# Optimization experiments

Hardware: AMD Instinct MI355X
Metric: run time of the kernel (lower is better)

## Reference

```python
import jax, jax.numpy as jnp
import numpy as np

B, L, K, S, D, H, C = 32, 256, 50, 16, 128, 4, 128
V, NN, NU, NS = 50000, 100000, 50000, 5000


def mha(q, k, v, in_w, in_b, out_w, out_b, n_heads):
    # PyTorch nn.MultiheadAttention (batch_first, eval mode) semantics.
    d = q.shape[-1]
    hd = d // n_heads
    wq, wk, wv = jnp.split(in_w, 3, axis=0)
    bq, bk, bv = jnp.split(in_b, 3)
    def heads(t):
        return t.reshape(t.shape[:-1] + (n_heads, hd))
    qh = heads(q @ wq.T + bq)
    kh = heads(k @ wk.T + bk)
    vh = heads(v @ wv.T + bv)
    scores = jnp.einsum('...qhd,...khd->...hqk', qh, kh) / jnp.sqrt(jnp.asarray(hd, q.dtype))
    attn = jax.nn.softmax(scores, axis=-1)
    o = jnp.einsum('...hqk,...khd->...qhd', attn, vh)
    o = o.reshape(o.shape[:-2] + (d,))
    return o @ out_w.T + out_b


def conv1d(x, w, b):
    # x: [B, D, L], w: [Cout, D, k]
    y = jax.lax.conv_general_dilated(x, w, (1,), 'VALID', dimension_numbers=('NCH', 'OIH', 'NCH'))
    return y + b[None, :, None]


def meta_path_module(paths, gru_wih, gru_whh, gru_bih, gru_bhh, in_w, in_b, out_w, out_b, ln_g, ln_b):
    # paths: [B, S, T, D] -> [B, D]
    b, s, t, d = paths.shape
    x = paths.reshape(b * s, t, d)
    def step(h, xt):
        gi = xt @ gru_wih.T + gru_bih
        gh = h @ gru_whh.T + gru_bhh
        ir, iz, inn = jnp.split(gi, 3, axis=-1)
        hr, hz, hn = jnp.split(gh, 3, axis=-1)
        r = jax.nn.sigmoid(ir + hr)
        z = jax.nn.sigmoid(iz + hz)
        n = jnp.tanh(inn + r * hn)
        return (1.0 - z) * n + z * h, None
    h0 = jnp.zeros((b * s, d), paths.dtype)
    h, _ = jax.lax.scan(step, h0, jnp.swapaxes(x, 0, 1))
    enc = h.reshape(b, s, d)
    attn = mha(enc, enc, enc, in_w, in_b, out_w, out_b, H)
    y = enc + attn
    mu = jnp.mean(y, -1, keepdims=True)
    var = jnp.var(y, -1, keepdims=True)
    y = (y - mu) / jnp.sqrt(var + 1e-5) * ln_g + ln_b
    return jnp.mean(y, axis=1)


def _forward(word_table, news_table, user_table, source_table,
             wa_in_w, wa_in_b, wa_out_w, wa_out_b,
             conv_w3, conv_b3, conv_w4, conv_b4, conv_w5, conv_b5, fc_w, fc_b,
             nsn_gru_wih, nsn_gru_whh, nsn_gru_bih, nsn_gru_bhh,
             nsn_in_w, nsn_in_b, nsn_out_w, nsn_out_b, nsn_ln_g, nsn_ln_b,
             nun_gru_wih, nun_gru_whh, nun_gru_bih, nun_gru_bhh,
             nun_in_w, nun_in_b, nun_out_w, nun_out_b, nun_ln_g, nun_ln_b,
             mp_w1, mp_b1, mp_w2, mp_b2, cls_w1, cls_b1, cls_w2, cls_b2,
             news_ids, news_word_indices, word_ctx_ids, nsn_src, nsn_end, nun_usr, nun_end):
    # --- fine-grained word embeds: per-token query attending over context news ---
    base = word_table[news_word_indices]              # [B, L, D]
    ctx = news_table[word_ctx_ids]                    # [B, L, K, D] (dominant gather)
    q = base[:, :, None, :]                           # [B, L, 1, D]
    fine = mha(q, ctx, ctx, wa_in_w, wa_in_b, wa_out_w, wa_out_b, H)[:, :, 0, :]
    pad = (news_word_indices == 0)[..., None]
    doc = jnp.where(pad, jnp.zeros((), base.dtype), fine)   # padding_idx=0 -> zeros
    # --- coarse CNN encoder ---
    x = jnp.swapaxes(doc, 1, 2)                       # [B, D, L]
    pooled = [jnp.max(jax.nn.relu(conv1d(x, w, b)), axis=2)
              for w, b in ((conv_w3, conv_b3), (conv_w4, conv_b4), (conv_w5, conv_b5))]
    semantic = jnp.concatenate(pooled, axis=1) @ fc_w.T + fc_b   # [B, D]
    # --- meta-path interaction ---
    start = jnp.broadcast_to(news_table[news_ids][:, None, :], (B, S, D))
    nsn_paths = jnp.stack([start, source_table[nsn_src], news_table[nsn_end]], axis=2)
    nun_paths = jnp.stack([start, user_table[nun_usr], news_table[nun_end]], axis=2)
    nsn_e = meta_path_module(nsn_paths, nsn_gru_wih, nsn_gru_whh, nsn_gru_bih, nsn_gru_bhh,
                             nsn_in_w, nsn_in_b, nsn_out_w, nsn_out_b, nsn_ln_g, nsn_ln_b)
    nun_e = meta_path_module(nun_paths, nun_gru_wih, nun_gru_whh, nun_gru_bih, nun_gru_bhh,
                             nun_in_w, nun_in_b, nun_out_w, nun_out_b, nun_ln_g, nun_ln_b)
    stack = jnp.stack([nsn_e, nun_e], axis=1)         # [B, 2, D]
    sc = jnp.tanh(stack @ mp_w1.T + mp_b1) @ mp_w2.T + mp_b2
    w = jax.nn.softmax(sc, axis=1)
    struct = jnp.sum(stack * w, axis=1)
    comb = jnp.concatenate([semantic, struct], axis=1)
    hcls = jax.nn.relu(comb @ cls_w1.T + cls_b1)
    return hcls @ cls_w2.T + cls_b2                   # [B, 2]


def setup_inputs() -> dict:
    key = jax.random.key(0)
    ks = iter(jax.random.split(key, 80))
    def p(shape):
        return (jax.random.normal(next(ks), shape, jnp.float32) * 0.02)
    inp = {}
    inp['news_ids'] = jax.random.randint(next(ks), (B,), 0, NN)
    inp['news_word_indices'] = jax.random.randint(next(ks), (B, L), 0, V)
    inp['word_ctx_ids'] = jax.random.randint(next(ks), (B, L, K), 0, NN)
    inp['nsn_src'] = jax.random.randint(next(ks), (B, S), 0, NS)
    inp['nsn_end'] = jax.random.randint(next(ks), (B, S), 0, NN)
    inp['nun_usr'] = jax.random.randint(next(ks), (B, S), 0, NU)
    inp['nun_end'] = jax.random.randint(next(ks), (B, S), 0, NN)
    inp['word_table'] = p((V, D)).at[0].set(0.0)
    inp['news_table'] = p((NN, D))
    inp['user_table'] = p((NU, D))
    inp['source_table'] = p((NS, D))
    inp['wa_in_w'] = p((3 * D, D)); inp['wa_in_b'] = p((3 * D,))
    inp['wa_out_w'] = p((D, D)); inp['wa_out_b'] = p((D,))
    for k in (3, 4, 5):
        inp[f'conv_w{k}'] = p((C, D, k)); inp[f'conv_b{k}'] = p((C,))
    inp['fc_w'] = p((D, 3 * C)); inp['fc_b'] = p((D,))
    for pre in ('nsn', 'nun'):
        inp[f'{pre}_gru_wih'] = p((3 * D, D)); inp[f'{pre}_gru_whh'] = p((3 * D, D))
        inp[f'{pre}_gru_bih'] = p((3 * D,)); inp[f'{pre}_gru_bhh'] = p((3 * D,))
        inp[f'{pre}_in_w'] = p((3 * D, D)); inp[f'{pre}_in_b'] = p((3 * D,))
        inp[f'{pre}_out_w'] = p((D, D)); inp[f'{pre}_out_b'] = p((D,))
        inp[f'{pre}_ln_g'] = jnp.ones((D,), jnp.float32); inp[f'{pre}_ln_b'] = jnp.zeros((D,), jnp.float32)
    inp['mp_w1'] = p((D // 2, D)); inp['mp_b1'] = p((D // 2,))
    inp['mp_w2'] = p((1, D // 2)); inp['mp_b2'] = p((1,))
    inp['cls_w1'] = p((D, 2 * D)); inp['cls_b1'] = p((D,))
    inp['cls_w2'] = p((2, D)); inp['cls_b2'] = p((2,))
    return inp


def reference(word_table, news_table, user_table, source_table,
              wa_in_w, wa_in_b, wa_out_w, wa_out_b,
              conv_w3, conv_b3, conv_w4, conv_b4, conv_w5, conv_b5, fc_w, fc_b,
              nsn_gru_wih, nsn_gru_whh, nsn_gru_bih, nsn_gru_bhh,
              nsn_in_w, nsn_in_b, nsn_out_w, nsn_out_b, nsn_ln_g, nsn_ln_b,
              nun_gru_wih, nun_gru_whh, nun_gru_bih, nun_gru_bhh,
              nun_in_w, nun_in_b, nun_out_w, nun_out_b, nun_ln_g, nun_ln_b,
              mp_w1, mp_b1, mp_w2, mp_b2, cls_w1, cls_b1, cls_w2, cls_b2,
              news_ids, news_word_indices, word_ctx_ids, nsn_src, nsn_end, nun_usr, nun_end):
    return _forward(word_table, news_table, user_table, source_table,
                    wa_in_w, wa_in_b, wa_out_w, wa_out_b,
                    conv_w3, conv_b3, conv_w4, conv_b4, conv_w5, conv_b5, fc_w, fc_b,
                    nsn_gru_wih, nsn_gru_whh, nsn_gru_bih, nsn_gru_bhh,
                    nsn_in_w, nsn_in_b, nsn_out_w, nsn_out_b, nsn_ln_g, nsn_ln_b,
                    nun_gru_wih, nun_gru_whh, nun_gru_bih, nun_gru_bhh,
                    nun_in_w, nun_in_b, nun_out_w, nun_out_b, nun_ln_g, nun_ln_b,
                    mp_w1, mp_b1, mp_w2, mp_b2, cls_w1, cls_b1, cls_w2, cls_b2,
                    news_ids, news_word_indices, word_ctx_ids, nsn_src, nsn_end, nun_usr, nun_end)
```

## Files before the change

### kernel.cpp

```cpp
#include <hip/hip_runtime.h>
#include <hip/hip_bf16.h>

#define BB 32
#define LL 256
#define KC 50
#define SS 16
#define DD 128
#define NH 4
#define CC 128
#define VV 50000
#define NNN 100000
#define NUU 50000
#define NSS 5000

typedef __attribute__((ext_vector_type(8))) short bf16x8;
typedef __attribute__((ext_vector_type(8))) unsigned short u16x8;
typedef __attribute__((ext_vector_type(4))) float f32x4;

__device__ __forceinline__ float dot4(float4 a, float4 b){
  return a.x*b.x + a.y*b.y + a.z*b.z + a.w*b.w;
}

__device__ __forceinline__ unsigned short f2bf(float f){
  union { float f; unsigned int u; } v; v.f = f;
  unsigned int r = (v.u + 0x7FFFu + ((v.u >> 16) & 1u)) >> 16;
  return (unsigned short)r;
}
__device__ __forceinline__ float bf2f(unsigned short s){
  union { unsigned int u; float f; } v; v.u = ((unsigned int)s) << 16;
  return v.f;
}

__global__ __launch_bounds__(256) void k_prep(
    const float* __restrict__ w3, const float* __restrict__ w4,
    const float* __restrict__ w5,
    const float* __restrict__ wih0, const float* __restrict__ whh0,
    const float* __restrict__ wih1, const float* __restrict__ whh1,
    const float* __restrict__ in_w, const float* __restrict__ out_w,
    const float* __restrict__ inw0, const float* __restrict__ outw0,
    const float* __restrict__ inw1, const float* __restrict__ outw1,
    unsigned short* __restrict__ wb3, unsigned short* __restrict__ wb4,
    unsigned short* __restrict__ wb5, unsigned short* __restrict__ wgb,
    unsigned short* __restrict__ wab, unsigned short* __restrict__ wmh){
  int e = blockIdx.x*256 + threadIdx.x;
  if (e < CC*DD*3){ int c=e/(DD*3), rm=e%(DD*3), d=rm/3, jj=rm%3;
    wb3[((size_t)jj*CC + c)*DD + d] = f2bf(w3[e]); }
  if (e < CC*DD*4){ int c=e/(DD*4), rm=e%(DD*4), d=rm/4, jj=rm%4;
    wb4[((size_t)jj*CC + c)*DD + d] = f2bf(w4[e]); }
  if (e < CC*DD*5){ int c=e/(DD*5), rm=e%(DD*5), d=rm/5, jj=rm%5;
    wb5[((size_t)jj*CC + c)*DD + d] = f2bf(w5[e]); }
  if (e < 384*DD){
    wgb[e]          = f2bf(wih0[e]);
    wgb[49152 + e]  = f2bf(whh0[e]);
    wgb[98304 + e]  = f2bf(wih1[e]);
    wgb[147456 + e] = f2bf(whh1[e]);
    wab[e]          = f2bf(in_w[e]);
  }
  if (e >= 384*DD && e < 512*DD) wab[e] = f2bf(out_w[e - 384*DD]);
  if (e < 512*DD){
    float s0 = (e < 384*DD) ? inw0[e] : outw0[e - 384*DD];
    float s1 = (e < 384*DD) ? inw1[e] : outw1[e - 384*DD];
    wmh[e]                 = f2bf(s0);
    wmh[(size_t)512*DD + e] = f2bf(s1);
  }
}

#define F1_GRU 128
#define F1_PKV 1250
#define PST 136
#define TST 72
#define CPAD 136
#define GSTR 392
__global__ __launch_bounds__(256) void k_fused1(
    const float* __restrict__ news, const unsigned short* __restrict__ wkvb,
    const float* __restrict__ in_b,
    unsigned short* __restrict__ nK, unsigned short* __restrict__ nV,
    const float* __restrict__ word_table, const int* __restrict__ widx,
    const unsigned short* __restrict__ wqb, float* __restrict__ qh_out,
    const float* __restrict__ user_table, const float* __restrict__ source_table,
    const int* __restrict__ news_ids, const int* __restrict__ nsn_src,
    const int* __restrict__ nsn_end, const int* __restrict__ nun_usr,
    const int* __restrict__ nun_end, const unsigned short* __restrict__ wgb,
    const float* __restrict__ bih0, const float* __restrict__ bhh0,
    const float* __restrict__ bih1, const float* __restrict__ bhh1,
    float* __restrict__ enc){
  __shared__ __align__(16) char smem[38912];
  const int blk = blockIdx.x;
  const int tid = threadIdx.x;
  const int wave = tid >> 6, lane = tid & 63, l15 = lane & 15, quad = lane >> 4;

  if (blk < F1_GRU){
    auto xs = (unsigned short(*)[CPAD])(smem);
    auto hs = (unsigned short(*)[CPAD])(smem + 4352);
    auto hf = (float(*)[128])(smem + 8704);
    auto gi = (float(*)[GSTR])(smem + 12800);
    auto gh = (float(*)[GSTR])(smem + 25344);
    const int m  = blk >> 6;
    const int b  = (blk >> 1) & 31;
    const int s0 = (blk & 1) * 8;
    const unsigned short* Wih = wgb + (size_t)m*2*384*DD;
    const unsigned short* Whh = Wih + 384*DD;
    const float* bih = m ? bih1 : bih0;
    const float* bhh = m ? bhh1 : bhh0;
    for (int i=tid;i<16*CPAD;i+=256){ (&xs[0][0])[i]=0; (&hs[0][0])[i]=0; }
    for (int i=tid;i<8*128;i+=256) (&hf[0][0])[i]=0.f;
    __syncthreads();
    for (int t=0;t<3;t++){
      {
        int s = tid >> 5, j = tid & 31;
        int row; const float* tab;
        if (t==0){ row = news_ids[b]; tab = news; }
        else if (t==1){ row = m ? nun_usr[b*SS+s0+s] : nsn_src[b*SS+s0+s];
                        tab = m ? user_table : source_table; }
        else { row = m ? nun_end[b*SS+s0+s] : nsn_end[b*SS+s0+s]; tab = news; }
        float4 v = ((const float4*)(tab + (size_t)row*DD))[j];
        unsigned short* dp = &xs[s][j*4];
        dp[0]=f2bf(v.x); dp[1]=f2bf(v.y); dp[2]=f2bf(v.z); dp[3]=f2bf(v.w);
      }
      __syncthreads();
      bf16x8 ax[4], ah[4];
      #pragma unroll
      for (int ks=0;ks<4;ks++){
        ax[ks] = *(const bf16x8*)&xs[l15][ks*32+quad*8];
        ah[ks] = *(const bf16x8*)&hs[l15][ks*32+quad*8];
      }
      #pragma unroll
      for (int nt=0;nt<6;nt++){
        const int n0 = wave*96 + nt*16;
        f32x4 ga = {0.f,0.f,0.f,0.f}, ha = {0.f,0.f,0.f,0.f};
        #pragma unroll
        for (int ks=0;ks<4;ks++){
          bf16x8 bi = *(const bf16x8*)(Wih + (size_t)(n0+l15)*DD + ks*32+quad*8);
          ga = __builtin_amdgcn_mfma_f32_16x16x32_bf16(ax[ks], bi, ga, 0,0,0);
          bf16x8 bh = *(const bf16x8*)(Whh + (size_t)(n0+l15)*DD + ks*32+quad*8);
          ha = __builtin_amdgcn_mfma_f32_16x16x32_bf16(ah[ks], bh, ha, 0,0,0);
        }
        if (quad < 2){
          #pragma unroll
          for (int r=0;r<4;r++){
            gi[quad*4+r][n0+l15] = ga[r];
            gh[quad*4+r][n0+l15] = ha[r];
          }
        }
      }
      __syncthreads();
      #pragma unroll
      for (int k=0;k<4;k++){
        int it = tid + k*256;
        int s = it >> 7, g = it & 127;
        float rr = 1.f/(1.f+__expf(-(gi[s][g] + gh[s][g] + bih[g] + bhh[g])));
        float zz = 1.f/(1.f+__expf(-(gi[s][128+g] + gh[s][128+g] + bih[128+g] + bhh[128+g])));
        float nn = tanhf(gi[s][256+g] + bih[256+g] + rr*(gh[s][256+g] + bhh[256+g]));
        float hnew = (1.f-zz)*nn + zz*hf[s][g];
        hf[s][g] = hnew;
        hs[s][g] = f2bf(hnew);
      }
      __syncthreads();
    }
    {
      int s = tid >> 5, j = tid & 31;
      float4 v = ((const float4*)hf[s])[j];
      ((float4*)(enc + (((size_t)m*BB + b)*SS + (s0+s))*DD))[j] = v;
    }
  } else if (blk < F1_GRU + F1_PKV){
    unsigned short* As = (unsigned short*)smem;
    unsigned short* Tw = (unsigned short*)(smem + 21760);
    const int r0 = (blk - F1_GRU) * 80;
    const int cw = wave * 64;
    bf16x8 wfr[4][4];
    #pragma unroll
    for (int nt=0; nt<4; nt++)
      #pragma unroll
      for (int ks=0; ks<4; ks++)
        wfr[nt][ks] = *(const bf16x8*)(wkvb + (size_t)(cw + nt*16 + l15)*DD + ks*32 + quad*8);
    float4 bv[4];
    #pragma unroll
    for (int nt=0; nt<4; nt++)
      bv[nt] = *(const float4*)(in_b + 128 + cw + nt*16 + quad*4);
    for (int i = tid; i < 80*32; i += 256){
      int row = i >> 5, j = i & 31;
      float4 v = ((const float4*)(news + (size_t)(r0 + row)*DD))[j];
      unsigned short* d = As + row*PST + j*4;
      d[0]=f2bf(v.x); d[1]=f2bf(v.y); d[2]=f2bf(v.z); d[3]=f2bf(v.w);
    }
    __syncthreads();
    unsigned short* outp = (wave < 2) ? nK : nV;
    const int cwo = (wave & 1) * 64;
    unsigned short* tw = Tw + wave*16*TST;
    const int rr = lane >> 4;
    const int cc = lane & 15;
    #pragma unroll
    for (int mt=0; mt<5; mt++){
      bf16x8 afr[4];
      #pragma unroll
      for (int ks=0; ks<4; ks++)
        afr[ks] = *(const bf16x8*)(As + (mt*16 + l15)*PST + ks*32 + quad*8);
      f32x4 acc[4];
      #pragma unroll
      for (int nt=0; nt<4; nt++) acc[nt] = (f32x4){0.f,0.f,0.f,0.f};
      #pragma unroll
      for (int ks=0; ks<4; ks++)
        #pragma unroll
        for (int nt=0; nt<4; nt++)
          acc[nt] = __builtin_amdgcn_mfma_f32_16x16x32_bf16(wfr[nt][ks], afr[ks], acc[nt], 0,0,0);
      #pragma unroll
      for (int nt=0; nt<4; nt++){
        unsigned short pk[4];
        pk[0] = f2bf(acc[nt][0] + bv[nt].x);
        pk[1] = f2bf(acc[nt][1] + bv[nt].y);
        pk[2] = f2bf(acc[nt][2] + bv[nt].z);
        pk[3] = f2bf(acc[nt][3] + bv[nt].w);
        *(unsigned long long*)(tw + l15*TST + nt*16 + quad*4) = *(const unsigned long long*)pk;
      }
      const int gr0 = r0 + mt*16;
      #pragma unroll
      for (int s=0; s<4; s++){
        unsigned long long v = *(const unsigned long long*)(tw + (s*4 + rr)*TST + cc*4);
        *(unsigned long long*)(outp + (size_t)(gr0 + s*4 + rr)*DD + cwo + cc*4) = v;
      }
    }
  } else {
    const int p0 = ((blk - F1_GRU - F1_PKV)*4 + wave) * 16;
    const int row = widx[p0 + l15];
    const float* src = word_table + (size_t)row*DD + quad*8;
    bf16x8 afr[4];
    #pragma unroll
    for (int ks=0; ks<4; ks++){
      float4 v0 = *(const float4*)(src + ks*32);
      float4 v1 = *(const float4*)(src + ks*32 + 4);
      bf16x8 a;
      a[0]=(short)f2bf(v0.x); a[1]=(short)f2bf(v0.y); a[2]=(short)f2bf(v0.z); a[3]=(short)f2bf(v0.w);
      a[4]=(short)f2bf(v1.x); a[5]=(short)f2bf(v1.y); a[6]=(short)f2bf(v1.z); a[7]=(short)f2bf(v1.w);
      afr[ks] = a;
    }
    #pragma unroll
    for (int nt=0; nt<8; nt++){
      const int n0 = nt*16;
      bf16x8 bfr[4];
      #pragma unroll
      for (int ks=0; ks<4; ks++)
        bfr[ks] = *(const bf16x8*)(wqb + (size_t)(n0+l15)*DD + ks*32 + quad*8);
      const float bias = in_b[n0 + l15];
      f32x4 acc = {0.f,0.f,0.f,0.f};
      #pragma unroll
      for (int ks=0; ks<4; ks++)
        acc = __builtin_amdgcn_mfma_f32_16x16x32_bf16(afr[ks], bfr[ks], acc, 0,0,0);
      #pragma unroll
      for (int r=0;r<4;r++){
        int m = quad*4 + r;
        qh_out[(size_t)(p0+m)*DD + n0 + l15] = acc[r] + bias;
      }
    }
  }
}

__global__ __launch_bounds__(64) void k_attn(
    const float* __restrict__ qh, const unsigned short* __restrict__ nK,
    const unsigned short* __restrict__ nV, const int* __restrict__ ctx_ids,
    unsigned short* __restrict__ o_out){
  const int p = blockIdx.x;
  const int lane = threadIdx.x;
  const int r = lane >> 4;
  const int g = lane & 15;
  const int h = g >> 2;
  __shared__ int ids[52];
  __shared__ float sc[NH][52];
  if (lane < KC) ids[lane] = ctx_ids[(size_t)p*KC + lane];
  float qv[8];
  {
    const float4* qp = (const float4*)(qh + (size_t)p*DD + g*8);
    float4 q0 = qp[0], q1 = qp[1];
    qv[0]=q0.x; qv[1]=q0.y; qv[2]=q0.z; qv[3]=q0.w;
    qv[4]=q1.x; qv[5]=q1.y; qv[6]=q1.z; qv[7]=q1.w;
  }
  __syncthreads();
  for (int kb=0; kb<13; kb++){
    int k2 = kb*4 + r;
    int row = ids[(k2 < KC) ? k2 : 0];
    u16x8 kv = *(const u16x8*)(nK + (size_t)row*DD + g*8);
    float pr = 0.f;
    #pragma unroll
    for (int j=0;j<8;j++) pr += qv[j]*bf2f(kv[j]);
    pr += __shfl_xor(pr, 1, 64);
    pr += __shfl_xor(pr, 2, 64);
    if ((g & 3) == 0 && k2 < KC) sc[h][k2] = pr;
  }
  __syncthreads();
  {
    const int hh = lane >> 4, kc = lane & 15;
    const float scale = 0.17677669529663687f;
    float mx = -1e30f;
    #pragma unroll
    for (int q4=0;q4<4;q4++){ int k2=kc+q4*16; if (k2<KC) mx = fmaxf(mx, sc[hh][k2]); }
    mx = fmaxf(mx, __shfl_xor(mx, 1, 64));
    mx = fmaxf(mx, __shfl_xor(mx, 2, 64));
    mx = fmaxf(mx, __shfl_xor(mx, 4, 64));
    mx = fmaxf(mx, __shfl_xor(mx, 8, 64));
    float sm = 0.f;
    float ev[4];
    #pragma unroll
    for (int q4=0;q4<4;q4++){
      int k2=kc+q4*16;
      ev[q4] = (k2<KC) ? __expf((sc[hh][k2]-mx)*scale) : 0.f;
      sm += ev[q4];
    }
    sm += __shfl_xor(sm, 1, 64);
    sm += __shfl_xor(sm, 2, 64);
    sm += __shfl_xor(sm, 4, 64);
    sm += __shfl_xor(sm, 8, 64);
    float inv = 1.f/sm;
    #pragma unroll
    for (int q4=0;q4<4;q4++){ int k2=kc+q4*16; if (k2<KC) sc[hh][k2] = ev[q4]*inv; }
  }
  __syncthreads();
  float acc[8];
  #pragma unroll
  for (int j=0;j<8;j++) acc[j]=0.f;
  for (int kb=0; kb<13; kb++){
    int k2 = kb*4 + r;
    int row = ids[(k2 < KC) ? k2 : 0];
    float w = (k2 < KC) ? sc[h][k2] : 0.f;
    u16x8 vv = *(const u16x8*)(nV + (size_t)row*DD + g*8);
    #pragma unroll
    for (int j=0;j<8;j++) acc[j] += w*bf2f(vv[j]);
  }
  #pragma unroll
  for (int j=0;j<8;j++){
    acc[j] += __shfl_xor(acc[j], 16, 64);
    acc[j] += __shfl_xor(acc[j], 32, 64);
  }
  if (r == 0){
    u16x8 o;
    #pragma unroll
    for (int j=0;j<8;j++) o[j] = f2bf(acc[j]);
    *(u16x8*)(o_out + (size_t)p*DD + g*8) = o;
  }
}

#define MPAD 136
__global__ __launch_bounds__(256) void k_fused2(
    const unsigned short* __restrict__ o_attn, const int* __restrict__ widx,
    const unsigned short* __restrict__ wob, const float* __restrict__ out_b,
    unsigned short* __restrict__ doc,
    const float* __restrict__ enc, const unsigned short* __restrict__ wmh,
    const float* __restrict__ inb0, const float* __restrict__ outb0,
    const float* __restrict__ lng0, const float* __restrict__ lnb0,
    const float* __restrict__ inb1, const float* __restrict__ outb1,
    const float* __restrict__ lng1, const float* __restrict__ lnb1,
    float* __restrict__ meta_e){
  __shared__ __align__(16) char smem[39296];
  const int blk = blockIdx.x;
  const int tid = threadIdx.x;
  const int wave = tid >> 6, lane = tid & 63, l15 = lane & 15, quad = lane >> 4;

  if (blk < 128){
    const int p0 = (blk*4 + wave) * 16;
    bf16x8 afr[4];
    #pragma unroll
    for (int ks=0; ks<4; ks++)
      afr[ks] = *(const bf16x8*)(o_attn + (size_t)(p0+l15)*DD + ks*32 + quad*8);
    int msk[4];
    #pragma unroll
    for (int r=0;r<4;r++) msk[r] = widx[p0 + quad*4 + r];
    #pragma unroll
    for (int nt=0; nt<8; nt++){
      const int n0 = nt*16;
      bf16x8 bfr[4];
      #pragma unroll
      for (int ks=0; ks<4; ks++)
        bfr[ks] = *(const bf16x8*)(wob + (size_t)(n0+l15)*DD + ks*32 + quad*8);
      const float bias = out_b[n0 + l15];
      f32x4 acc = {0.f,0.f,0.f,0.f};
      #pragma unroll
      for (int ks=0; ks<4; ks++)
        acc = __builtin_amdgcn_mfma_f32_16x16x32_bf16(afr[ks], bfr[ks], acc, 0,0,0);
      #pragma unroll
      for (int r=0;r<4;r++){
        int m = quad*4 + r;
        doc[(size_t)(p0+m)*DD + n0 + l15] = (msk[r] == 0) ? (unsigned short)0
                                                          : f2bf(acc[r] + bias);
      }
    }
  } else {
    auto ebf = (unsigned short(*)[MPAD])(smem);
    auto qb  = (unsigned short(*)[MPAD])(smem + 4352);
    auto kb  = (unsigned short(*)[MPAD])(smem + 8704);
    auto ob  = (unsigned short(*)[MPAD])(smem + 13056);
    auto vf  = (float(*)[128])(smem + 17408);
    auto er  = (float(*)[132])(smem + 25600);
    auto at  = (float(*)[16][16])(smem + 34048);
    float* mu = (float*)(smem + 38144);
    float* rs = (float*)(smem + 38208);
    auto part = (float(*)[128])(smem + 38272);
    const int mb = blk - 128;
    const int m = mb >> 5;
    const int b = mb & 31;
    const unsigned short* W = wmh + (size_t)m*512*DD;
    const float* in_b  = m ? inb1 : inb0;
    const float* outb  = m ? outb1 : outb0;
    const float* lng   = m ? lng1 : lng0;
    const float* lnb   = m ? lnb1 : lnb0;
    const float* esrc = enc + ((size_t)m*BB + b)*SS*DD;
    for (int i = tid; i < 16*32; i += 256){
      int s = i >> 5, j = i & 31;
      float4 v = ((const float4*)esrc)[i];
      ((float4*)er[s])[j] = v;
      unsigned short* dp = &ebf[s][j*4];
      dp[0]=f2bf(v.x); dp[1]=f2bf(v.y); dp[2]=f2bf(v.z); dp[3]=f2bf(v.w);
    }
    __syncthreads();
    {
      bf16x8 ax[4];
      #pragma unroll
      for (int ks=0;ks<4;ks++) ax[ks] = *(const bf16x8*)&ebf[l15][ks*32+quad*8];
      #pragma unroll
      for (int nt=0; nt<6; nt++){
        const int n0 = wave*96 + nt*16;
        f32x4 acc = {0.f,0.f,0.f,0.f};
        #pragma unroll
        for (int ks=0;ks<4;ks++){
          bf16x8 bw = *(const bf16x8*)(W + (size_t)(n0+l15)*DD + ks*32+quad*8);
          acc = __builtin_amdgcn_mfma_f32_16x16x32_bf16(ax[ks], bw, acc, 0,0,0);
        }
        const float bias = in_b[n0+l15];
        const int col = n0 + l15;
        #pragma unroll
        for (int r=0;r<4;r++){
          int row = quad*4+r;
          float val = acc[r] + bias;
          if (n0 < 128)      qb[row][col]       = f2bf(val);
          else if (n0 < 256) kb[row][col-128]   = f2bf(val);
          else               vf[row][col-256]   = val;
        }
      }
    }
    __syncthreads();
    {
      const int h = wave;
      bf16x8 aq = *(const bf16x8*)&qb[l15][h*32 + quad*8];
      bf16x8 ak = *(const bf16x8*)&kb[l15][h*32 + quad*8];
      f32x4 z = {0.f,0.f,0.f,0.f};
      f32x4 acc = __builtin_amdgcn_mfma_f32_16x16x32_bf16(aq, ak, z, 0,0,0);
      #pragma unroll
      for (int r=0;r<4;r++)
        at[h][quad*4+r][l15] = acc[r] * 0.17677669529663687f;
    }
    __syncthreads();
    if (tid < 64){
      int h = tid>>4, qi = tid&15;
      float mx=-1e30f;
      #pragma unroll
      for (int ki=0;ki<16;ki++) mx = fmaxf(mx, at[h][qi][ki]);
      float sm=0.f;
      float ee[16];
      #pragma unroll
      for (int ki=0;ki<16;ki++){ ee[ki]=__expf(at[h][qi][ki]-mx); sm+=ee[ki]; }
      float inv=1.f/sm;
      #pragma unroll
      for (int ki=0;ki<16;ki++) at[h][qi][ki]=ee[ki]*inv;
    }
    __syncthreads();
    {
      int c = tid & 127, h = c >> 5;
      int sBase = (tid >> 7) * 8;
      #pragma unroll
      for (int s=0;s<8;s++){
        float acc=0.f;
        #pragma unroll
        for (int ki=0;ki<16;ki++) acc += at[h][sBase+s][ki]*vf[ki][c];
        ob[sBase+s][c] = f2bf(acc);
// ... 122 lines not shown
  }
}

__global__ __launch_bounds__(128) void k_final(
    const float* __restrict__ convp,
    const float* __restrict__ cb3, const float* __restrict__ cb4,
    const float* __restrict__ cb5,
    const float* __restrict__ fc_w, const float* __restrict__ fc_b,
    const float* __restrict__ meta_e,
    const float* __restrict__ mp_w1, const float* __restrict__ mp_b1,
    const float* __restrict__ mp_w2, const float* __restrict__ mp_b2,
    const float* __restrict__ cls_w1, const float* __restrict__ cls_b1,
    const float* __restrict__ cls_w2, const float* __restrict__ cls_b2,
    float* __restrict__ out){
  const int b = blockIdx.x;
  const int c = threadIdx.x;
  __shared__ float pooled[384];
  __shared__ float comb[256];
  __shared__ float hcls[128];
  __shared__ float tt[2][64];
  __shared__ float wsc[2];
  for (int idx=c; idx<384; idx+=128){
    int j = idx >> 7, cc2 = idx & 127;
    const float* base = convp + (((size_t)b*3 + j)*4)*CC + cc2;
    float mx = -1e30f;
    for (int ci=0;ci<4;ci++) mx = fmaxf(mx, base[ci*CC]);
    const float* cb = (j==0)?cb3:(j==1)?cb4:cb5;
    pooled[idx] = fmaxf(mx + cb[cc2], 0.f);
  }
  __syncthreads();
  {
    float acc = fc_b[c];
    const float* wr = fc_w + (size_t)c*384;
    for (int i=0;i<384;i++) acc += pooled[i]*wr[i];
    comb[c] = acc;
  }
  if (c < 64){
    for (int m=0;m<2;m++){
      const float* ev = meta_e + ((size_t)m*BB+b)*DD;
      float acc = mp_b1[c];
      const float* wr = mp_w1 + (size_t)c*DD;
      for (int i=0;i<DD;i++) acc += ev[i]*wr[i];
      tt[m][c] = tanhf(acc);
    }
  }
  __syncthreads();
  if (c == 0){
    float s0 = mp_b2[0], s1 = mp_b2[0];
    for (int j=0;j<64;j++){ s0 += tt[0][j]*mp_w2[j]; s1 += tt[1][j]*mp_w2[j]; }
    float mx = fmaxf(s0,s1);
    float e0 = __expf(s0-mx), e1 = __expf(s1-mx);
    wsc[0] = e0/(e0+e1); wsc[1] = e1/(e0+e1);
  }
  __syncthreads();
  comb[128+c] = wsc[0]*meta_e[((size_t)b)*DD + c]
              + wsc[1]*meta_e[((size_t)(BB+b))*DD + c];
  __syncthreads();
  {
    float acc = cls_b1[c];
    const float* wr = cls_w1 + (size_t)c*256;
    for (int i=0;i<256;i++) acc += comb[i]*wr[i];
    hcls[c] = fmaxf(acc, 0.f);
  }
  __syncthreads();
  if (c < 2){
    float acc = cls_b2[c];
    const float* wr = cls_w2 + (size_t)c*DD;
    for (int i=0;i<DD;i++) acc += hcls[i]*wr[i];
    out[b*2 + c] = acc;
  }
}

extern "C" void kernel_launch(void* const* d_in, const int* in_sizes, int n_in,
                              void* d_out, int out_size, void* d_ws, size_t ws_size,
                              hipStream_t stream){
  const int* news_ids = (const int*)d_in[0];
  const int* nwi      = (const int*)d_in[1];
  const int* ctx_ids  = (const int*)d_in[2];
  const int* nsn_src  = (const int*)d_in[3];
  const int* nsn_end  = (const int*)d_in[4];
  const int* nun_usr  = (const int*)d_in[5];
  const int* nun_end  = (const int*)d_in[6];
  const float* word_table   = (const float*)d_in[7];
  const float* news_table   = (const float*)d_in[8];
  const float* user_table   = (const float*)d_in[9];
  const float* source_table = (const float*)d_in[10];
  const float* wa_in_w  = (const float*)d_in[11];
  const float* wa_in_b  = (const float*)d_in[12];
  const float* wa_out_w = (const float*)d_in[13];
  const float* wa_out_b = (const float*)d_in[14];
  const float* conv_w3 = (const float*)d_in[15];
  const float* conv_b3 = (const float*)d_in[16];
  const float* conv_w4 = (const float*)d_in[17];
  const float* conv_b4 = (const float*)d_in[18];
  const float* conv_w5 = (const float*)d_in[19];
  const float* conv_b5 = (const float*)d_in[20];
  const float* fc_w = (const float*)d_in[21];
  const float* fc_b = (const float*)d_in[22];
  const float* wih0 = (const float*)d_in[23];
  const float* whh0 = (const float*)d_in[24];
  const float* bih0 = (const float*)d_in[25];
  const float* bhh0 = (const float*)d_in[26];
  const float* inw0 = (const float*)d_in[27];
  const float* inb0 = (const float*)d_in[28];
  const float* outw0 = (const float*)d_in[29];
  const float* outb0 = (const float*)d_in[30];
  const float* lng0 = (const float*)d_in[31];
  const float* lnb0 = (const float*)d_in[32];
  const float* wih1 = (const float*)d_in[33];
  const float* whh1 = (const float*)d_in[34];
  const float* bih1 = (const float*)d_in[35];
  const float* bhh1 = (const float*)d_in[36];
  const float* inw1 = (const float*)d_in[37];
  const float* inb1 = (const float*)d_in[38];
  const float* outw1 = (const float*)d_in[39];
  const float* outb1 = (const float*)d_in[40];
  const float* lng1 = (const float*)d_in[41];
  const float* lnb1 = (const float*)d_in[42];
  const float* mp_w1 = (const float*)d_in[43];
  const float* mp_b1 = (const float*)d_in[44];
  const float* mp_w2 = (const float*)d_in[45];
  const float* mp_b2 = (const float*)d_in[46];
  const float* cls_w1 = (const float*)d_in[47];
  const float* cls_b1 = (const float*)d_in[48];
  const float* cls_w2 = (const float*)d_in[49];
  const float* cls_b2 = (const float*)d_in[50];

  char* wsb = (char*)d_ws;
  unsigned short* nK = (unsigned short*)wsb;
  unsigned short* nV = nK + (size_t)NNN*DD;
  unsigned short* wb3 = nV + (size_t)NNN*DD;
  unsigned short* wb4 = wb3 + (size_t)CC*DD*3;
  unsigned short* wb5 = wb4 + (size_t)CC*DD*4;
  unsigned short* wgb = wb5 + (size_t)CC*DD*5;
  unsigned short* wab = wgb + (size_t)4*384*DD;
  unsigned short* wmh = wab + (size_t)512*DD;
  float* qh     = (float*)(wmh + (size_t)2*512*DD);
  unsigned short* o_at = (unsigned short*)(qh + (size_t)BB*LL*DD);
  unsigned short* doc  = (unsigned short*)((float*)o_at + (size_t)BB*LL*DD);
  float* convp  = (float*)doc + (size_t)BB*LL*DD;
  float* enc    = convp + BB*3*4*CC;
  float* meta_e = enc + (size_t)2*BB*SS*DD;
  const size_t need_bytes = (size_t)((char*)(meta_e + 2*BB*DD) - wsb);
  if (ws_size < need_bytes) return;

  const unsigned short* wqb  = wab;
  const unsigned short* wkvb = wab + (size_t)128*DD;
  const unsigned short* wob  = wab + (size_t)384*DD;

  k_prep<<<dim3(320), dim3(256), 0, stream>>>(conv_w3, conv_w4, conv_w5,
      wih0, whh0, wih1, whh1, wa_in_w, wa_out_w,
      inw0, outw0, inw1, outw1,
      wb3, wb4, wb5, wgb, wab, wmh);
  k_fused1<<<dim3(F1_GRU + F1_PKV + 128), dim3(256), 0, stream>>>(
      news_table, wkvb, wa_in_b, nK, nV,
      word_table, nwi, wqb, qh,
      user_table, source_table, news_ids, nsn_src, nsn_end, nun_usr, nun_end,
      wgb, bih0, bhh0, bih1, bhh1, enc);
  k_attn<<<dim3(BB*LL), dim3(64), 0, stream>>>(qh, nK, nV, ctx_ids, o_at);
  k_fused2<<<dim3(192), dim3(256), 0, stream>>>(o_at, nwi, wob, wa_out_b, doc,
      enc, wmh, inb0, outb0, lng0, lnb0, inb1, outb1, lng1, lnb1, meta_e);
  k_conv<<<dim3(BB*3*4), dim3(256), 0, stream>>>(doc, wb3, wb4, wb5, convp);
  k_final<<<dim3(BB), dim3(128), 0, stream>>>(convp, conv_b3, conv_b4, conv_b5,
      fc_w, fc_b, meta_e, mp_w1, mp_b1, mp_w2, mp_b2,
      cls_w1, cls_b1, cls_w2, cls_b2, (float*)d_out);
}
```

Before: 360.2 us.

## Split GRU out of fused projection kernel and shrink K/V projection register footprint

Moves the GRU meta-path blocks into a separate k_gru kernel, so the K/V/Q projection kernel no longer reserves the large shared buffer the GRU needs. The K/V projection now processes its 64 output columns in two 32-column halves, holding 8 weight fragments in registers instead of 16, with a smaller transpose staging buffer. Lower LDS and VGPR usage is meant to raise occupancy for the bandwidth-bound projection. The cost is an extra kernel launch and a serialized small GRU kernel, plus reloading weight fragments per half.

```diff
diff --git a/kernel.cpp b/kernel.cpp
--- a/kernel.cpp
+++ b/kernel.cpp
@@ -65,118 +65,23 @@
   }
 }
 
-#define F1_GRU 128
-#define F1_PKV 1250
+#define PQ_PKV 1250
 #define PST 136
-#define TST 72
-#define CPAD 136
-#define GSTR 392
-__global__ __launch_bounds__(256) void k_fused1(
+#define TST2 40
+__global__ __launch_bounds__(256) void k_pq(
     const float* __restrict__ news, const unsigned short* __restrict__ wkvb,
     const float* __restrict__ in_b,
     unsigned short* __restrict__ nK, unsigned short* __restrict__ nV,
     const float* __restrict__ word_table, const int* __restrict__ widx,
-    const unsigned short* __restrict__ wqb, float* __restrict__ qh_out,
-    const float* __restrict__ user_table, const float* __restrict__ source_table,
-    const int* __restrict__ news_ids, const int* __restrict__ nsn_src,
-    const int* __restrict__ nsn_end, const int* __restrict__ nun_usr,
-    const int* __restrict__ nun_end, const unsigned short* __restrict__ wgb,
-    const float* __restrict__ bih0, const float* __restrict__ bhh0,
-    const float* __restrict__ bih1, const float* __restrict__ bhh1,
-    float* __restrict__ enc){
-  __shared__ __align__(16) char smem[38912];
+    const unsigned short* __restrict__ wqb, float* __restrict__ qh_out){
+  __shared__ __align__(16) unsigned short As[80*PST];
+  __shared__ __align__(16) unsigned short Tw[4*16*TST2];
   const int blk = blockIdx.x;
   const int tid = threadIdx.x;
   const int wave = tid >> 6, lane = tid & 63, l15 = lane & 15, quad = lane >> 4;
 
-  if (blk < F1_GRU){
-    auto xs = (unsigned short(*)[CPAD])(smem);
-    auto hs = (unsigned short(*)[CPAD])(smem + 4352);
-    auto hf = (float(*)[128])(smem + 8704);
-    auto gi = (float(*)[GSTR])(smem + 12800);
-    auto gh = (float(*)[GSTR])(smem + 25344);
-    const int m  = blk >> 6;
-    const int b  = (blk >> 1) & 31;
-    const int s0 = (blk & 1) * 8;
-    const unsigned short* Wih = wgb + (size_t)m*2*384*DD;
-    const unsigned short* Whh = Wih + 384*DD;
-    const float* bih = m ? bih1 : bih0;
-    const float* bhh = m ? bhh1 : bhh0;
-    for (int i=tid;i<16*CPAD;i+=256){ (&xs[0][0])[i]=0; (&hs[0][0])[i]=0; }
-    for (int i=tid;i<8*128;i+=256) (&hf[0][0])[i]=0.f;
-    __syncthreads();
-    for (int t=0;t<3;t++){
-      {
-        int s = tid >> 5, j = tid & 31;
-        int row; const float* tab;
-        if (t==0){ row = news_ids[b]; tab = news; }
-        else if (t==1){ row = m ? nun_usr[b*SS+s0+s] : nsn_src[b*SS+s0+s];
-                        tab = m ? user_table : source_table; }
-        else { row = m ? nun_end[b*SS+s0+s] : nsn_end[b*SS+s0+s]; tab = news; }
-        float4 v = ((const float4*)(tab + (size_t)row*DD))[j];
-        unsigned short* dp = &xs[s][j*4];
-        dp[0]=f2bf(v.x); dp[1]=f2bf(v.y); dp[2]=f2bf(v.z); dp[3]=f2bf(v.w);
-      }
-      __syncthreads();
-      bf16x8 ax[4], ah[4];
-      #pragma unroll
-      for (int ks=0;ks<4;ks++){
-        ax[ks] = *(const bf16x8*)&xs[l15][ks*32+quad*8];
-        ah[ks] = *(const bf16x8*)&hs[l15][ks*32+quad*8];
-      }
-      #pragma unroll
-      for (int nt=0;nt<6;nt++){
-        const int n0 = wave*96 + nt*16;
-        f32x4 ga = {0.f,0.f,0.f,0.f}, ha = {0.f,0.f,0.f,0.f};
-        #pragma unroll
-        for (int ks=0;ks<4;ks++){
-          bf16x8 bi = *(const bf16x8*)(Wih + (size_t)(n0+l15)*DD + ks*32+quad*8);
-          ga = __builtin_amdgcn_mfma_f32_16x16x32_bf16(ax[ks], bi, ga, 0,0,0);
-          bf16x8 bh = *(const bf16x8*)(Whh + (size_t)(n0+l15)*DD + ks*32+quad*8);
-          ha = __builtin_amdgcn_mfma_f32_16x16x32_bf16(ah[ks], bh, ha, 0,0,0);
-        }
-        if (quad < 2){
-          #pragma unroll
-          for (int r=0;r<4;r++){
-            gi[quad*4+r][n0+l15] = ga[r];
-            gh[quad*4+r][n0+l15] = ha[r];
-          }
-        }
-      }
-      __syncthreads();
-      #pragma unroll
-      for (int k=0;k<4;k++){
-        int it = tid + k*256;
-        int s = it >> 7, g = it & 127;
-        float rr = 1.f/(1.f+__expf(-(gi[s][g] + gh[s][g] + bih[g] + bhh[g])));
-        float zz = 1.f/(1.f+__expf(-(gi[s][128+g] + gh[s][128+g] + bih[128+g] + bhh[128+g])));
-        float nn = tanhf(gi[s][256+g] + bih[256+g] + rr*(gh[s][256+g] + bhh[256+g]));
-        float hnew = (1.f-zz)*nn + zz*hf[s][g];
-        hf[s][g] = hnew;
-        hs[s][g] = f2bf(hnew);
-      }
-      __syncthreads();
-    }
-    {
-      int s = tid >> 5, j = tid & 31;
-      float4 v = ((const float4*)hf[s])[j];
-      ((float4*)(enc + (((size_t)m*BB + b)*SS + (s0+s))*DD))[j] = v;
-    }
-  } else if (blk < F1_GRU + F1_PKV){
-    unsigned short* As = (unsigned short*)smem;
-    unsigned short* Tw = (unsigned short*)(smem + 21760);
-    const int r0 = (blk - F1_GRU) * 80;
-    const int cw = wave * 64;
-    bf16x8 wfr[4][4];
-    #pragma unroll
-    for (int nt=0; nt<4; nt++)
-      #pragma unroll
-      for (int ks=0; ks<4; ks++)
-        wfr[nt][ks] = *(const bf16x8*)(wkvb + (size_t)(cw + nt*16 + l15)*DD + ks*32 + quad*8);
-    float4 bv[4];
-    #pragma unroll
-    for (int nt=0; nt<4; nt++)
-      bv[nt] = *(const float4*)(in_b + 128 + cw + nt*16 + quad*4);
+  if (blk < PQ_PKV){
+    const int r0 = blk * 80;
     for (int i = tid; i < 80*32; i += 256){
       int row = i >> 5, j = i & 31;
       float4 v = ((const float4*)(news + (size_t)(r0 + row)*DD))[j];
@@ -185,42 +90,50 @@
     }
     __syncthreads();
     unsigned short* outp = (wave < 2) ? nK : nV;
-    const int cwo = (wave & 1) * 64;
-    unsigned short* tw = Tw + wave*16*TST;
-    const int rr = lane >> 4;
-    const int cc = lane & 15;
-    #pragma unroll
-    for (int mt=0; mt<5; mt++){
-      bf16x8 afr[4];
-      #pragma unroll
-      for (int ks=0; ks<4; ks++)
-        afr[ks] = *(const bf16x8*)(As + (mt*16 + l15)*PST + ks*32 + quad*8);
-      f32x4 acc[4];
-      #pragma unroll
-      for (int nt=0; nt<4; nt++) acc[nt] = (f32x4){0.f,0.f,0.f,0.f};
-      #pragma unroll
-      for (int ks=0; ks<4; ks++)
-        #pragma unroll
-        for (int nt=0; nt<4; nt++)
-          acc[nt] = __builtin_amdgcn_mfma_f32_16x16x32_bf16(wfr[nt][ks], afr[ks], acc[nt], 0,0,0);
-      #pragma unroll
-      for (int nt=0; nt<4; nt++){
-        unsigned short pk[4];
-        pk[0] = f2bf(acc[nt][0] + bv[nt].x);
-        pk[1] = f2bf(acc[nt][1] + bv[nt].y);
-        pk[2] = f2bf(acc[nt][2] + bv[nt].z);
-        pk[3] = f2bf(acc[nt][3] + bv[nt].w);
-        *(unsigned long long*)(tw + l15*TST + nt*16 + quad*4) = *(const unsigned long long*)pk;
-      }
-      const int gr0 = r0 + mt*16;
-      #pragma unroll
-      for (int s=0; s<4; s++){
-        unsigned long long v = *(const unsigned long long*)(tw + (s*4 + rr)*TST + cc*4);
-        *(unsigned long long*)(outp + (size_t)(gr0 + s*4 + rr)*DD + cwo + cc*4) = v;
+    unsigned short* tw = Tw + wave*16*TST2;
+    const int rr8 = lane >> 3, cc8 = lane & 7;
+    for (int half=0; half<2; half++){
+      const int c0 = wave*64 + half*32;
+      const int cm = c0 & 127;
+      bf16x8 wfr[2][4];
+      #pragma unroll
+      for (int nt=0; nt<2; nt++)
+        #pragma unroll
+        for (int ks=0; ks<4; ks++)
+          wfr[nt][ks] = *(const bf16x8*)(wkvb + (size_t)(c0 + nt*16 + l15)*DD + ks*32 + quad*8);
+      float4 bv0 = *(const float4*)(in_b + 128 + c0 + quad*4);
+      float4 bv1 = *(const float4*)(in_b + 128 + c0 + 16 + quad*4);
+      #pragma unroll
+      for (int mt=0; mt<5; mt++){
+        bf16x8 afr[4];
+        #pragma unroll
+        for (int ks=0; ks<4; ks++)
+          afr[ks] = *(const bf16x8*)(As + (mt*16 + l15)*PST + ks*32 + quad*8);
+        f32x4 a0 = {0.f,0.f,0.f,0.f}, a1 = {0.f,0.f,0.f,0.f};
+        #pragma unroll
+        for (int ks=0; ks<4; ks++){
+          a0 = __builtin_amdgcn_mfma_f32_16x16x32_bf16(wfr[0][ks], afr[ks], a0, 0,0,0);
+          a1 = __builtin_amdgcn_mfma_f32_16x16x32_bf16(wfr[1][ks], afr[ks], a1, 0,0,0);
+        }
+        {
+          unsigned short pk[4];
+          pk[0]=f2bf(a0[0]+bv0.x); pk[1]=f2bf(a0[1]+bv0.y);
+          pk[2]=f2bf(a0[2]+bv0.z); pk[3]=f2bf(a0[3]+bv0.w);
+          *(unsigned long long*)(tw + l15*TST2 + quad*4) = *(const unsigned long long*)pk;
+          pk[0]=f2bf(a1[0]+bv1.x); pk[1]=f2bf(a1[1]+bv1.y);
+          pk[2]=f2bf(a1[2]+bv1.z); pk[3]=f2bf(a1[3]+bv1.w);
+          *(unsigned long long*)(tw + l15*TST2 + 16 + quad*4) = *(const unsigned long long*)pk;
+        }
+        const int gr0 = r0 + mt*16;
+        #pragma unroll
+        for (int s=0; s<2; s++){
+          unsigned long long v = *(const unsigned long long*)(tw + (s*8+rr8)*TST2 + cc8*4);
+          *(unsigned long long*)(outp + (size_t)(gr0 + s*8 + rr8)*DD + cm + cc8*4) = v;
+        }
       }
     }
   } else {
-    const int p0 = ((blk - F1_GRU - F1_PKV)*4 + wave) * 16;
+    const int p0 = ((blk - PQ_PKV)*4 + wave) * 16;
     const int row = widx[p0 + l15];
     const float* src = word_table + (size_t)row*DD + quad*8;
     bf16x8 afr[4];
@@ -251,6 +164,95 @@
         qh_out[(size_t)(p0+m)*DD + n0 + l15] = acc[r] + bias;
       }
     }
+  }
+}
+
+#define CPAD 136
+#define GSTR 392
+__global__ __launch_bounds__(256) void k_gru(
+    const float* __restrict__ news_table, const float* __restrict__ user_table,
+    const float* __restrict__ source_table,
+    const int* __restrict__ news_ids, const int* __restrict__ nsn_src,
+    const int* __restrict__ nsn_end, const int* __restrict__ nun_usr,
+    const int* __restrict__ nun_end,
+    const unsigned short* __restrict__ wgb,
+    const float* __restrict__ bih0, const float* __restrict__ bhh0,
+    const float* __restrict__ bih1, const float* __restrict__ bhh1,
+    float* __restrict__ enc){
+  __shared__ __align__(16) unsigned short xs[16][CPAD];
+  __shared__ __align__(16) unsigned short hs[16][CPAD];
+  __shared__ float hf[8][128];
+  __shared__ float gi[8][GSTR];
+  __shared__ float gh[8][GSTR];
+  const int blk = blockIdx.x;
+  const int m  = blk >> 6;
+  const int b  = (blk >> 1) & 31;
+  const int s0 = (blk & 1) * 8;
+  const int tid = threadIdx.x;
+  const int wave = tid >> 6, lane = tid & 63, l15 = lane & 15, quad = lane >> 4;
+  const unsigned short* Wih = wgb + (size_t)m*2*384*DD;
+  const unsigned short* Whh = Wih + 384*DD;
+  const float* bih = m ? bih1 : bih0;
+  const float* bhh = m ? bhh1 : bhh0;
+  for (int i=tid;i<16*CPAD;i+=256){ (&xs[0][0])[i]=0; (&hs[0][0])[i]=0; }
+  for (int i=tid;i<8*128;i+=256) (&hf[0][0])[i]=0.f;
+  __syncthreads();
+  for (int t=0;t<3;t++){
+    {
+      int s = tid >> 5, j = tid & 31;
+      int row; const float* tab;
+      if (t==0){ row = news_ids[b]; tab = news_table; }
+      else if (t==1){ row = m ? nun_usr[b*SS+s0+s] : nsn_src[b*SS+s0+s];
+                      tab = m ? user_table : source_table; }
+      else { row = m ? nun_end[b*SS+s0+s] : nsn_end[b*SS+s0+s]; tab = news_table; }
+      float4 v = ((const float4*)(tab + (size_t)row*DD))[j];
+      unsigned short* dp = &xs[s][j*4];
+      dp[0]=f2bf(v.x); dp[1]=f2bf(v.y); dp[2]=f2bf(v.z); dp[3]=f2bf(v.w);
+    }
+    __syncthreads();
+    bf16x8 ax[4], ah[4];
+    #pragma unroll
+    for (int ks=0;ks<4;ks++){
+      ax[ks] = *(const bf16x8*)&xs[l15][ks*32+quad*8];
+      ah[ks] = *(const bf16x8*)&hs[l15][ks*32+quad*8];
+    }
+    #pragma unroll
+    for (int nt=0;nt<6;nt++){
+      const int n0 = wave*96 + nt*16;
+      f32x4 ga = {0.f,0.f,0.f,0.f}, ha = {0.f,0.f,0.f,0.f};
+      #pragma unroll
+      for (int ks=0;ks<4;ks++){
+        bf16x8 bi = *(const bf16x8*)(Wih + (size_t)(n0+l15)*DD + ks*32+quad*8);
+        ga = __builtin_amdgcn_mfma_f32_16x16x32_bf16(ax[ks], bi, ga, 0,0,0);
+        bf16x8 bh = *(const bf16x8*)(Whh + (size_t)(n0+l15)*DD + ks*32+quad*8);
+        ha = __builtin_amdgcn_mfma_f32_16x16x32_bf16(ah[ks], bh, ha, 0,0,0);
+      }
+      if (quad < 2){
+        #pragma unroll
+        for (int r=0;r<4;r++){
+          gi[quad*4+r][n0+l15] = ga[r];
+          gh[quad*4+r][n0+l15] = ha[r];
+        }
+      }
+    }
+    __syncthreads();
+    #pragma unroll
+    for (int k=0;k<4;k++){
+      int it = tid + k*256;
+      int s = it >> 7, g = it & 127;
+      float rr = 1.f/(1.f+__expf(-(gi[s][g] + gh[s][g] + bih[g] + bhh[g])));
+      float zz = 1.f/(1.f+__expf(-(gi[s][128+g] + gh[s][128+g] + bih[128+g] + bhh[128+g])));
+      float nn = tanhf(gi[s][256+g] + bih[256+g] + rr*(gh[s][256+g] + bhh[256+g]));
+      float hnew = (1.f-zz)*nn + zz*hf[s][g];
+      hf[s][g] = hnew;
+      hs[s][g] = f2bf(hnew);
+    }
+    __syncthreads();
+  }
+  {
+    int s = tid >> 5, j = tid & 31;
+    float4 v = ((const float4*)hf[s])[j];
+    ((float4*)(enc + (((size_t)m*BB + b)*SS + (s0+s))*DD))[j] = v;
   }
 }
 
@@ -744,10 +746,11 @@
       wih0, whh0, wih1, whh1, wa_in_w, wa_out_w,
       inw0, outw0, inw1, outw1,
       wb3, wb4, wb5, wgb, wab, wmh);
-  k_fused1<<<dim3(F1_GRU + F1_PKV + 128), dim3(256), 0, stream>>>(
+  k_pq<<<dim3(PQ_PKV + 128), dim3(256), 0, stream>>>(
       news_table, wkvb, wa_in_b, nK, nV,
-      word_table, nwi, wqb, qh,
-      user_table, source_table, news_ids, nsn_src, nsn_end, nun_usr, nun_end,
+      word_table, nwi, wqb, qh);
+  k_gru<<<dim3(128), dim3(256), 0, stream>>>(news_table, user_table, source_table,
+      news_ids, nsn_src, nsn_end, nun_usr, nun_end,
       wgb, bih0, bhh0, bih1, bhh1, enc);
   k_attn<<<dim3(BB*LL), dim3(64), 0, stream>>>(qh, nK, nV, ctx_ids, o_at);
   k_fused2<<<dim3(192), dim3(256), 0, stream>>>(o_at, nwi, wob, wa_out_b, doc,
```

Result: faster. 352.6 us (-2.1%).

## Split GRU path out of fused projection kernel and unroll attention key loops

Applied to the files above, without the earlier changes.

Moves the GRU encoder blocks out of the fused K/V/Q projection kernel into a separate kernel, so the projection kernel only allocates the shared memory and registers its own path needs. The aim is higher occupancy for the 1378 projection blocks, which had been sized for the larger GRU shared-memory footprint. It also fully unrolls the two 13-iteration gather loops in the attention kernel to expose more independent loads. The cost is an extra kernel launch, and the GRU work no longer overlaps with the projection work inside one grid.

```diff
diff --git a/kernel.cpp b/kernel.cpp
--- a/kernel.cpp
+++ b/kernel.cpp
@@ -65,107 +65,23 @@
   }
 }
 
-#define F1_GRU 128
-#define F1_PKV 1250
+#define PQ_PKV 1250
 #define PST 136
 #define TST 72
-#define CPAD 136
-#define GSTR 392
-__global__ __launch_bounds__(256) void k_fused1(
+__global__ __launch_bounds__(256) void k_pq(
     const float* __restrict__ news, const unsigned short* __restrict__ wkvb,
     const float* __restrict__ in_b,
     unsigned short* __restrict__ nK, unsigned short* __restrict__ nV,
     const float* __restrict__ word_table, const int* __restrict__ widx,
-    const unsigned short* __restrict__ wqb, float* __restrict__ qh_out,
-    const float* __restrict__ user_table, const float* __restrict__ source_table,
-    const int* __restrict__ news_ids, const int* __restrict__ nsn_src,
-    const int* __restrict__ nsn_end, const int* __restrict__ nun_usr,
-    const int* __restrict__ nun_end, const unsigned short* __restrict__ wgb,
-    const float* __restrict__ bih0, const float* __restrict__ bhh0,
-    const float* __restrict__ bih1, const float* __restrict__ bhh1,
-    float* __restrict__ enc){
-  __shared__ __align__(16) char smem[38912];
+    const unsigned short* __restrict__ wqb, float* __restrict__ qh_out){
+  __shared__ __align__(16) unsigned short As[80*PST];
+  __shared__ __align__(16) unsigned short Tw[4*16*TST];
   const int blk = blockIdx.x;
   const int tid = threadIdx.x;
   const int wave = tid >> 6, lane = tid & 63, l15 = lane & 15, quad = lane >> 4;
 
-  if (blk < F1_GRU){
-    auto xs = (unsigned short(*)[CPAD])(smem);
-    auto hs = (unsigned short(*)[CPAD])(smem + 4352);
-    auto hf = (float(*)[128])(smem + 8704);
-    auto gi = (float(*)[GSTR])(smem + 12800);
-    auto gh = (float(*)[GSTR])(smem + 25344);
-    const int m  = blk >> 6;
-    const int b  = (blk >> 1) & 31;
-    const int s0 = (blk & 1) * 8;
-    const unsigned short* Wih = wgb + (size_t)m*2*384*DD;
-    const unsigned short* Whh = Wih + 384*DD;
-    const float* bih = m ? bih1 : bih0;
-    const float* bhh = m ? bhh1 : bhh0;
-    for (int i=tid;i<16*CPAD;i+=256){ (&xs[0][0])[i]=0; (&hs[0][0])[i]=0; }
-    for (int i=tid;i<8*128;i+=256) (&hf[0][0])[i]=0.f;
-    __syncthreads();
-    for (int t=0;t<3;t++){
-      {
-        int s = tid >> 5, j = tid & 31;
-        int row; const float* tab;
-        if (t==0){ row = news_ids[b]; tab = news; }
-        else if (t==1){ row = m ? nun_usr[b*SS+s0+s] : nsn_src[b*SS+s0+s];
-                        tab = m ? user_table : source_table; }
-        else { row = m ? nun_end[b*SS+s0+s] : nsn_end[b*SS+s0+s]; tab = news; }
-        float4 v = ((const float4*)(tab + (size_t)row*DD))[j];
-        unsigned short* dp = &xs[s][j*4];
-        dp[0]=f2bf(v.x); dp[1]=f2bf(v.y); dp[2]=f2bf(v.z); dp[3]=f2bf(v.w);
-      }
-      __syncthreads();
-      bf16x8 ax[4], ah[4];
-      #pragma unroll
-      for (int ks=0;ks<4;ks++){
-        ax[ks] = *(const bf16x8*)&xs[l15][ks*32+quad*8];
-        ah[ks] = *(const bf16x8*)&hs[l15][ks*32+quad*8];
-      }
-      #pragma unroll
-      for (int nt=0;nt<6;nt++){
-        const int n0 = wave*96 + nt*16;
-        f32x4 ga = {0.f,0.f,0.f,0.f}, ha = {0.f,0.f,0.f,0.f};
-        #pragma unroll
-        for (int ks=0;ks<4;ks++){
-          bf16x8 bi = *(const bf16x8*)(Wih + (size_t)(n0+l15)*DD + ks*32+quad*8);
-          ga = __builtin_amdgcn_mfma_f32_16x16x32_bf16(ax[ks], bi, ga, 0,0,0);
-          bf16x8 bh = *(const bf16x8*)(Whh + (size_t)(n0+l15)*DD + ks*32+quad*8);
-          ha = __builtin_amdgcn_mfma_f32_16x16x32_bf16(ah[ks], bh, ha, 0,0,0);
-        }
-        if (quad < 2){
-          #pragma unroll
-          for (int r=0;r<4;r++){
-            gi[quad*4+r][n0+l15] = ga[r];
-            gh[quad*4+r][n0+l15] = ha[r];
-          }
-        }
-      }
-      __syncthreads();
-      #pragma unroll
-      for (int k=0;k<4;k++){
-        int it = tid + k*256;
-        int s = it >> 7, g = it & 127;
-        float rr = 1.f/(1.f+__expf(-(gi[s][g] + gh[s][g] + bih[g] + bhh[g])));
-        float zz = 1.f/(1.f+__expf(-(gi[s][128+g] + gh[s][128+g] + bih[128+g] + bhh[128+g])));
-        float nn = tanhf(gi[s][256+g] + bih[256+g] + rr*(gh[s][256+g] + bhh[256+g]));
-        float hnew = (1.f-zz)*nn + zz*hf[s][g];
-        hf[s][g] = hnew;
-        hs[s][g] = f2bf(hnew);
-      }
-      __syncthreads();
-    }
-    {
-      int s = tid >> 5, j = tid & 31;
-      float4 v = ((const float4*)hf[s])[j];
-      ((float4*)(enc + (((size_t)m*BB + b)*SS + (s0+s))*DD))[j] = v;
-    }
-  } else if (blk < F1_GRU + F1_PKV){
-    unsigned short* As = (unsigned short*)smem;
-    unsigned short* Tw = (unsigned short*)(smem + 21760);
-    const int r0 = (blk - F1_GRU) * 80;
+  if (blk < PQ_PKV){
+    const int r0 = blk * 80;
     const int cw = wave * 64;
     bf16x8 wfr[4][4];
     #pragma unroll
@@ -220,7 +136,7 @@
       }
     }
   } else {
-    const int p0 = ((blk - F1_GRU - F1_PKV)*4 + wave) * 16;
+    const int p0 = ((blk - PQ_PKV)*4 + wave) * 16;
     const int row = widx[p0 + l15];
     const float* src = word_table + (size_t)row*DD + quad*8;
     bf16x8 afr[4];
@@ -251,6 +167,95 @@
         qh_out[(size_t)(p0+m)*DD + n0 + l15] = acc[r] + bias;
       }
     }
+  }
+}
+
+#define CPAD 136
+#define GSTR 392
+__global__ __launch_bounds__(256) void k_gru(
+    const float* __restrict__ news_table, const float* __restrict__ user_table,
+    const float* __restrict__ source_table,
+    const int* __restrict__ news_ids, const int* __restrict__ nsn_src,
+    const int* __restrict__ nsn_end, const int* __restrict__ nun_usr,
+    const int* __restrict__ nun_end,
+    const unsigned short* __restrict__ wgb,
+    const float* __restrict__ bih0, const float* __restrict__ bhh0,
+    const float* __restrict__ bih1, const float* __restrict__ bhh1,
+    float* __restrict__ enc){
+  __shared__ __align__(16) unsigned short xs[16][CPAD];
+  __shared__ __align__(16) unsigned short hs[16][CPAD];
+  __shared__ float hf[8][128];
+  __shared__ float gi[8][GSTR];
+  __shared__ float gh[8][GSTR];
+  const int blk = blockIdx.x;
+  const int m  = blk >> 6;
+  const int b  = (blk >> 1) & 31;
+  const int s0 = (blk & 1) * 8;
+  const int tid = threadIdx.x;
+  const int wave = tid >> 6, lane = tid & 63, l15 = lane & 15, quad = lane >> 4;
+  const unsigned short* Wih = wgb + (size_t)m*2*384*DD;
+  const unsigned short* Whh = Wih + 384*DD;
+  const float* bih = m ? bih1 : bih0;
+  const float* bhh = m ? bhh1 : bhh0;
+  for (int i=tid;i<16*CPAD;i+=256){ (&xs[0][0])[i]=0; (&hs[0][0])[i]=0; }
+  for (int i=tid;i<8*128;i+=256) (&hf[0][0])[i]=0.f;
+  __syncthreads();
+  for (int t=0;t<3;t++){
+    {
+      int s = tid >> 5, j = tid & 31;
+      int row; const float* tab;
+      if (t==0){ row = news_ids[b]; tab = news_table; }
+      else if (t==1){ row = m ? nun_usr[b*SS+s0+s] : nsn_src[b*SS+s0+s];
+                      tab = m ? user_table : source_table; }
+      else { row = m ? nun_end[b*SS+s0+s] : nsn_end[b*SS+s0+s]; tab = news_table; }
+      float4 v = ((const float4*)(tab + (size_t)row*DD))[j];
+      unsigned short* dp = &xs[s][j*4];
+      dp[0]=f2bf(v.x); dp[1]=f2bf(v.y); dp[2]=f2bf(v.z); dp[3]=f2bf(v.w);
+    }
+    __syncthreads();
+    bf16x8 ax[4], ah[4];
+    #pragma unroll
+    for (int ks=0;ks<4;ks++){
+      ax[ks] = *(const bf16x8*)&xs[l15][ks*32+quad*8];
+      ah[ks] = *(const bf16x8*)&hs[l15][ks*32+quad*8];
+    }
+    #pragma unroll
+    for (int nt=0;nt<6;nt++){
+      const int n0 = wave*96 + nt*16;
+      f32x4 ga = {0.f,0.f,0.f,0.f}, ha = {0.f,0.f,0.f,0.f};
+      #pragma unroll
+      for (int ks=0;ks<4;ks++){
+        bf16x8 bi = *(const bf16x8*)(Wih + (size_t)(n0+l15)*DD + ks*32+quad*8);
+        ga = __builtin_amdgcn_mfma_f32_16x16x32_bf16(ax[ks], bi, ga, 0,0,0);
+        bf16x8 bh = *(const bf16x8*)(Whh + (size_t)(n0+l15)*DD + ks*32+quad*8);
+        ha = __builtin_amdgcn_mfma_f32_16x16x32_bf16(ah[ks], bh, ha, 0,0,0);
+      }
+      if (quad < 2){
+        #pragma unroll
+        for (int r=0;r<4;r++){
+          gi[quad*4+r][n0+l15] = ga[r];
+          gh[quad*4+r][n0+l15] = ha[r];
+        }
+      }
+    }
+    __syncthreads();
+    #pragma unroll
+    for (int k=0;k<4;k++){
+      int it = tid + k*256;
+      int s = it >> 7, g = it & 127;
+      float rr = 1.f/(1.f+__expf(-(gi[s][g] + gh[s][g] + bih[g] + bhh[g])));
+      float zz = 1.f/(1.f+__expf(-(gi[s][128+g] + gh[s][128+g] + bih[128+g] + bhh[128+g])));
+      float nn = tanhf(gi[s][256+g] + bih[256+g] + rr*(gh[s][256+g] + bhh[256+g]));
+      float hnew = (1.f-zz)*nn + zz*hf[s][g];
+      hf[s][g] = hnew;
+      hs[s][g] = f2bf(hnew);
+    }
+    __syncthreads();
+  }
+  {
+    int s = tid >> 5, j = tid & 31;
+    float4 v = ((const float4*)hf[s])[j];
+    ((float4*)(enc + (((size_t)m*BB + b)*SS + (s0+s))*DD))[j] = v;
   }
 }
 
@@ -274,6 +279,7 @@
     qv[4]=q1.x; qv[5]=q1.y; qv[6]=q1.z; qv[7]=q1.w;
   }
   __syncthreads();
+  #pragma unroll
   for (int kb=0; kb<13; kb++){
     int k2 = kb*4 + r;
     int row = ids[(k2 < KC) ? k2 : 0];
@@ -316,6 +322,7 @@
   float acc[8];
   #pragma unroll
   for (int j=0;j<8;j++) acc[j]=0.f;
+  #pragma unroll
   for (int kb=0; kb<13; kb++){
     int k2 = kb*4 + r;
     int row = ids[(k2 < KC) ? k2 : 0];
@@ -744,10 +751,11 @@
       wih0, whh0, wih1, whh1, wa_in_w, wa_out_w,
       inw0, outw0, inw1, outw1,
       wb3, wb4, wb5, wgb, wab, wmh);
-  k_fused1<<<dim3(F1_GRU + F1_PKV + 128), dim3(256), 0, stream>>>(
+  k_pq<<<dim3(PQ_PKV + 128), dim3(256), 0, stream>>>(
       news_table, wkvb, wa_in_b, nK, nV,
-      word_table, nwi, wqb, qh,
-      user_table, source_table, news_ids, nsn_src, nsn_end, nun_usr, nun_end,
+      word_table, nwi, wqb, qh);
+  k_gru<<<dim3(128), dim3(256), 0, stream>>>(news_table, user_table, source_table,
+      news_ids, nsn_src, nsn_end, nun_usr, nun_end,
       wgb, bih0, bhh0, bih1, bhh1, enc);
   k_attn<<<dim3(BB*LL), dim3(64), 0, stream>>>(qh, nK, nV, ctx_ids, o_at);
   k_fused2<<<dim3(192), dim3(256), 0, stream>>>(o_at, nwi, wob, wa_out_b, doc,
```

New measurement: 351.6 us. 1.02x faster.
